# Kernel optimization log

Measured on AMD Instinct MI355X. Metric: run time of the kernel, lower is better.

The kernel has to match this reference:

```python
import jax, jax.numpy as jnp
import numpy as np

GAMMA = 0.99
LMBDA = 0.95
SHAPE = (8192, 256, 4, 1)  # (batch, steps, agents, 1)


def setup_inputs() -> dict:
    key = jax.random.key(0)
    k1, k2, k3, k4 = jax.random.split(key, 4)
    reward = jax.random.normal(k1, SHAPE, dtype=jnp.float32)
    # sparse binary termination flags (as float, matching terminated.float())
    terminated = (jax.random.uniform(k2, SHAPE) < 0.01).astype(jnp.float32)
    value = jax.random.normal(k3, SHAPE, dtype=jnp.float32)
    next_value = jax.random.normal(k4, SHAPE, dtype=jnp.float32)
    return {"reward": reward, "terminated": terminated,
            "value": value, "next_value": next_value}


def _gae(reward, terminated, value, next_value):
    not_done = 1.0 - terminated
    # delta_t = r_t + gamma * V(s_{t+1}) * not_done_t - V(s_t), all steps at once
    delta = reward + GAMMA * next_value * not_done - value  # (B, T, ...)

    # time-major for the scan: (T, B, ...)
    delta_t = jnp.moveaxis(delta, 1, 0)
    nd_t = jnp.moveaxis(not_done, 1, 0)

    def step(gae, x):
        d, nd = x
        gae = d + GAMMA * LMBDA * nd * gae
        return gae, gae

    init = jnp.zeros(delta_t.shape[1:], dtype=delta.dtype)
    # reverse=True: backward-time recurrence, outputs aligned to original order
    _, adv_t = jax.lax.scan(step, init, (delta_t, nd_t), reverse=True)
    advantages = jnp.moveaxis(adv_t, 0, 1)  # back to (B, T, ...)
    returns = advantages + value
    return advantages, returns


def reference(reward, terminated, value, next_value):
    return _gae(reward, terminated, value, next_value)
```

## Files before the change

kernel.cpp:

```cpp
#include <hip/hip_runtime.h>


#define GAMMA 0.99f
#define LMBDA 0.95f

constexpr int T = 256;

__global__ __launch_bounds__(256, 4) void gae_scan_kernel(
    const float* __restrict__ reward,
    const float* __restrict__ terminated,
    const float* __restrict__ value,
    const float* __restrict__ next_value,
    float* __restrict__ adv_out,
    float* __restrict__ ret_out)
{
    const int lane = threadIdx.x & 63;
    const int b    = (blockIdx.x * blockDim.x + threadIdx.x) >> 6;
    const int tc   = lane >> 2;
    const int a    = lane & 3;

    const int base = b * 1024 + 1020 - 64 * tc + a;

    float d[16], c[16], vv[16];
#pragma unroll
    for (int j = 0; j < 16; ++j) {
        const int o = base - 4 * j;
        const float r  = reward[o];
        const float tm = terminated[o];
        const float v  = value[o];
        const float nv = next_value[o];
        const float nd = 1.0f - tm;
        d[j]  = r + GAMMA * nv * nd - v;
        c[j]  = (GAMMA * LMBDA) * nd;
        vv[j] = v;
    }

    float D = d[0], K = c[0];
#pragma unroll
    for (int j = 1; j < 16; ++j) { D = d[j] + c[j] * D; K = c[j] * K; }

#pragma unroll
    for (int s = 1; s < 16; s <<= 1) {
        const float pD = __shfl_up(D, (unsigned)(s * 4), 64);
        const float pK = __shfl_up(K, (unsigned)(s * 4), 64);
        if (tc >= s) { D = D + K * pD; K = K * pK; }
    }

    float x = __shfl_up(D, 4u, 64);
    if (tc == 0) x = 0.0f;

    float g = x;
#pragma unroll
    for (int j = 0; j < 16; ++j) {
        g = d[j] + c[j] * g;
        const int o = base - 4 * j;
        adv_out[o] = g;
        ret_out[o] = g + vv[j];
    }
}

extern "C" void kernel_launch(void* const* d_in, const int* in_sizes, int n_in,
                              void* d_out, int out_size, void* d_ws, size_t ws_size,
                              hipStream_t stream) {
    const float* reward     = (const float*)d_in[0];
    const float* terminated = (const float*)d_in[1];
    const float* value      = (const float*)d_in[2];
    const float* next_value = (const float*)d_in[3];

    const int B = 8192;
    const int n_elem = B * T * 4;
    float* adv = (float*)d_out;
    float* ret = adv + n_elem;

    const int blocks = (B * 64) / 256;
    gae_scan_kernel<<<blocks, 256, 0, stream>>>(reward, terminated, value,
                                                next_value, adv, ret);
}
```

Before: 211.6 us.

## Stage GAE tiles through LDS with coalesced float4 loads and stores

Each wave now loads its batch row with contiguous float4 global loads, computes delta and decay coefficients, and writes them into a swizzled shared-memory layout. The existing per-lane segmented scan then reads from LDS. Results go back to LDS and are written out as coalesced float4 stores. This replaces strided scalar global accesses with vectorized coalesced ones, at the cost of LDS traffic, two block barriers and more shared memory per block. Launch bounds are also raised to request higher occupancy.

```diff
diff --git a/kernel.cpp b/kernel.cpp
--- a/kernel.cpp
+++ b/kernel.cpp
@@ -6,7 +6,7 @@
 
 constexpr int T = 256;
 
-__global__ __launch_bounds__(256, 4) void gae_scan_kernel(
+__global__ __launch_bounds__(256, 5) void gae_scan_kernel(
     const float* __restrict__ reward,
     const float* __restrict__ terminated,
     const float* __restrict__ value,
@@ -14,25 +14,55 @@
     float* __restrict__ adv_out,
     float* __restrict__ ret_out)
 {
+    __shared__ float bufD[4][16 * 64];
+    __shared__ float bufC[4][16 * 64];
+
+    const int w    = threadIdx.x >> 6;
     const int lane = threadIdx.x & 63;
-    const int b    = (blockIdx.x * blockDim.x + threadIdx.x) >> 6;
-    const int tc   = lane >> 2;
-    const int a    = lane & 3;
+    const int b    = blockIdx.x * 4 + w;
 
-    const int base = b * 1024 + 1020 - 64 * tc + a;
+    float* __restrict__ D_ = bufD[w];
+    float* __restrict__ C_ = bufC[w];
 
-    float d[16], c[16], vv[16];
+    float4 v4[4];
+#pragma unroll
+    for (int q = 0; q < 4; ++q) {
+        const int f  = 64 * q + lane;
+        const int gi = b * 256 + f;
+        const float4 r  = ((const float4*)reward)[gi];
+        const float4 tm = ((const float4*)terminated)[gi];
+        const float4 v  = ((const float4*)value)[gi];
+        const float4 nv = ((const float4*)next_value)[gi];
+        v4[q] = v;
+
+        const int s    = 255 - f;
+        const int row  = s & 15;
+        const int col  = (4 * (s >> 4) + 4 * row) & 63;
+        const int addr = row * 64 + col;
+
+        float4 d4, c4;
+        d4.x = r.x + GAMMA * nv.x * (1.0f - tm.x) - v.x;
+        d4.y = r.y + GAMMA * nv.y * (1.0f - tm.y) - v.y;
+        d4.z = r.z + GAMMA * nv.z * (1.0f - tm.z) - v.z;
+        d4.w = r.w + GAMMA * nv.w * (1.0f - tm.w) - v.w;
+        c4.x = (GAMMA * LMBDA) * (1.0f - tm.x);
+        c4.y = (GAMMA * LMBDA) * (1.0f - tm.y);
+        c4.z = (GAMMA * LMBDA) * (1.0f - tm.z);
+        c4.w = (GAMMA * LMBDA) * (1.0f - tm.w);
+        *((float4*)&D_[addr]) = d4;
+        *((float4*)&C_[addr]) = c4;
+    }
+    __syncthreads();
+
+    const int tc = lane >> 2;
+    const int a  = lane & 3;
+
+    float d[16], c[16];
 #pragma unroll
     for (int j = 0; j < 16; ++j) {
-        const int o = base - 4 * j;
-        const float r  = reward[o];
-        const float tm = terminated[o];
-        const float v  = value[o];
-        const float nv = next_value[o];
-        const float nd = 1.0f - tm;
-        d[j]  = r + GAMMA * nv * nd - v;
-        c[j]  = (GAMMA * LMBDA) * nd;
-        vv[j] = v;
+        const int col = (4 * tc + 4 * j + a) & 63;
+        d[j] = D_[j * 64 + col];
+        c[j] = C_[j * 64 + col];
     }
 
     float D = d[0], K = c[0];
@@ -40,10 +70,10 @@
     for (int j = 1; j < 16; ++j) { D = d[j] + c[j] * D; K = c[j] * K; }
 
 #pragma unroll
-    for (int s = 1; s < 16; s <<= 1) {
-        const float pD = __shfl_up(D, (unsigned)(s * 4), 64);
-        const float pK = __shfl_up(K, (unsigned)(s * 4), 64);
-        if (tc >= s) { D = D + K * pD; K = K * pK; }
+    for (int s2 = 1; s2 < 16; s2 <<= 1) {
+        const float pD = __shfl_up(D, (unsigned)(4 * s2), 64);
+        const float pK = __shfl_up(K, (unsigned)(4 * s2), 64);
+        if (tc >= s2) { D = D + K * pD; K = K * pK; }
     }
 
     float x = __shfl_up(D, 4u, 64);
@@ -53,9 +83,27 @@
 #pragma unroll
     for (int j = 0; j < 16; ++j) {
         g = d[j] + c[j] * g;
-        const int o = base - 4 * j;
-        adv_out[o] = g;
-        ret_out[o] = g + vv[j];
+        const int col = (4 * tc + 4 * j + a) & 63;
+        D_[j * 64 + col] = g;
+    }
+    __syncthreads();
+
+#pragma unroll
+    for (int q = 0; q < 4; ++q) {
+        const int f   = 64 * q + lane;
+        const int s   = 255 - f;
+        const int row = s & 15;
+        const int col = (4 * (s >> 4) + 4 * row) & 63;
+        const float4 g4 = *((const float4*)&D_[row * 64 + col]);
+
+        const int gi = b * 256 + f;
+        ((float4*)adv_out)[gi] = g4;
+        float4 rt;
+        rt.x = g4.x + v4[q].x;
+        rt.y = g4.y + v4[q].y;
+        rt.z = g4.z + v4[q].z;
+        rt.w = g4.w + v4[q].w;
+        ((float4*)ret_out)[gi] = rt;
     }
 }
 
@@ -72,7 +120,6 @@
     float* adv = (float*)d_out;
     float* ret = adv + n_elem;
 
-    const int blocks = (B * 64) / 256;
-    gae_scan_kernel<<<blocks, 256, 0, stream>>>(reward, terminated, value,
-                                                next_value, adv, ret);
+    gae_scan_kernel<<<B / 4, 256, 0, stream>>>(reward, terminated, value,
+                                               next_value, adv, ret);
 }
```

Measured after the change: 179.1 us. 15.4% less time.
